# Kernel tuning notes

Hardware: AMD Instinct MI355X
Metric: run time of the kernel (lower is better)

The kernel has to match this reference:

```python
import jax, jax.numpy as jnp
import numpy as np

T, D, N, K, V = 4, 1024, 256, 64, 32000
SGLD_A, SGLD_B, SGLD_C = 0.01, 1.0, 0.55
PHI_VAR, ETA_VAR = 1.0, 1.0
ZERO = 1e-6

def jax_exp(x):
    return jnp.clip(jnp.exp(jnp.clip(x, -700.0, 700.0)), ZERO)

def setup_inputs() -> dict:
    key = jax.random.key(0)
    ks = jax.random.split(key, 13)
    W = jax.random.randint(ks[0], (T, D, N), 0, V, dtype=jnp.int32)
    Z = jax.random.randint(ks[1], (T, D, N), 0, K - 1, dtype=jnp.int32)
    prop_word_idx = jax.random.randint(ks[2], (T, D, N), 0, N, dtype=jnp.int32)
    prop_topic = jax.random.randint(ks[3], (T, D, N), 0, K - 1, dtype=jnp.int32)
    u_mh = jax.random.uniform(ks[4], (T, D, N, 2), dtype=jnp.float32)
    noise_eta = jax.random.normal(ks[5], (T, D), dtype=jnp.float32)
    noise_phi = jax.random.normal(ks[6], (T,), dtype=jnp.float32)
    alpha = jax.random.normal(ks[7], (T, K), dtype=jnp.float32)
    phi = jax.random.normal(ks[8], (T, V, K), dtype=jnp.float32) * 0.1
    eta = jax.random.normal(ks[9], (T, D, K), dtype=jnp.float32) * 0.1
    CDK = jax.random.uniform(ks[10], (T, D, K), dtype=jnp.float32) * (N / K)
    CWK = jax.random.uniform(ks[11], (T, V, K), dtype=jnp.float32)
    CK = jax.random.uniform(ks[12], (T, K), dtype=jnp.float32) * (D * N / K)
    return dict(W=W, Z=Z, prop_word_idx=prop_word_idx, prop_topic=prop_topic,
                u_mh=u_mh, noise_eta=noise_eta, noise_phi=noise_phi,
                alpha=alpha, phi=phi, eta=eta, CDK=CDK, CWK=CWK, CK=CK)

def reference(W, Z, prop_word_idx, prop_topic, u_mh, noise_eta, noise_phi,
              alpha, phi, eta, CDK, CWK, CK):
    eps = SGLD_A * (SGLD_B + 0.0) ** (-SGLD_C)  # SGLD step at iteration 0

    # --- SGLD update of eta (per doc), vmapped over (T, D) via broadcasting ---
    prior_eta = (alpha[:, None, :] - eta) / ETA_VAR                 # [T,D,K]
    grad_eta = CDK - N * jax.nn.softmax(eta, axis=-1)               # [T,D,K]
    eta_new = eta + eps / 2 * (grad_eta + prior_eta) + noise_eta[..., None] * eps

    tt = jnp.arange(T)[:, None, None]   # [T,1,1]
    dd = jnp.arange(D)[None, :, None]   # [1,D,1]

    # --- MH step 1: word-proposal (acceptance via phi ratio) ---
    pre = Z                                                           # [T,D,N]
    prop1 = jnp.take_along_axis(Z, prop_word_idx, axis=2)             # [T,D,N]
    a1 = jax_exp(phi[tt, W, prop1]) / jax_exp(phi[tt, W, pre])
    k1 = jnp.where(u_mh[..., 0] < a1, prop1, pre)

    # --- MH step 2: topic-proposal (acceptance via eta ratio) ---
    a2 = jax_exp(eta_new[tt, dd, prop_topic]) / jax_exp(eta_new[tt, dd, k1])
    z_new = jnp.where(u_mh[..., 1] < a2, prop_topic, k1)              # [T,D,N]

    # --- scatter counter updates (add new assignment, remove old) ---
    CDK_new = CDK.at[tt, dd, z_new].add(1.0).at[tt, dd, Z].add(-1.0)
    CWK_new = CWK.at[tt, W, z_new].add(1.0).at[tt, W, Z].add(-1.0)
    CK_new = CK.at[tt, z_new].add(1.0).at[tt, Z].add(-1.0)

    # --- SGLD update of phi: sequential over T (reads updated phi[t-1]) ---
    rows = [phi[t] for t in range(T)]   # each [V,K]
    phi_sigma = 1.0 / (1.0 / 100.0 + 1.0 / PHI_VAR)
    for t in range(T):
        if t == 0:
            prior = (2.0 * phi[1] * (phi_sigma / PHI_VAR) - 2.0 * rows[0]) / PHI_VAR
        elif t == T - 1:
            prior = (rows[t - 1] - rows[t]) / PHI_VAR
        else:
            prior = (phi[t + 1] + rows[t - 1] - 2.0 * rows[t]) / PHI_VAR
        grad = CWK_new[t] - CK_new[t][None, :] * jax.nn.softmax(rows[t], axis=0)
        rows[t] = rows[t] + eps / 2 * (grad + prior) + noise_phi[t] * eps
    phi_new = jnp.stack(rows)

    return (eta_new, phi_new, CDK_new, CWK_new, CK_new, z_new)
```

## Files before the change

### kernel.cpp

```cpp
#include <hip/hip_runtime.h>

#define T 4
#define D 1024
#define NN 256
#define K 64
#define V 32000
#define VK (V*K)
#define TD (T*D)

__device__ __forceinline__ float jexp(float x) {
    x = fminf(fmaxf(x, -700.0f), 700.0f);
    return fmaxf(expf(x), 1e-6f);
}


__global__ void fused_kernel(const int* __restrict__ W, const int* __restrict__ Z,
                             const int* __restrict__ pwi, const int* __restrict__ ptop,
                             const float* __restrict__ u, const float* __restrict__ phi,
                             const float* __restrict__ eta,
                             const float* __restrict__ alpha,
                             const float* __restrict__ noise_eta,
                             const float* __restrict__ CDK,
                             const float* __restrict__ CK,
                             float* __restrict__ S_part,
                             float* __restrict__ CK_new,
                             float* __restrict__ eta_new,
                             float* __restrict__ CDK_new,
                             unsigned int* __restrict__ plus,
                             unsigned int* __restrict__ minus,
                             float* __restrict__ z_out)
{
    int blk = blockIdx.x;
    int n = threadIdx.x;

    __shared__ float sm[256];
    __shared__ float esh[K];
    __shared__ int   hist[K];

    if (blk < 500) {
        if (blk == 0) CK_new[n] = CK[n];
        int t = blk / 125;
        int vbase = (blk % 125) * 256;
        int k = n & 63;
        int rr = n >> 6;
        const float* base = phi + (size_t)t * VK;
        float s = 0.0f;
        #pragma unroll 4
        for (int it = 0; it < 64; ++it) {
            int v = vbase + it * 4 + rr;
            s += expf(base[v * K + k]);
        }
        sm[n] = s;
        __syncthreads();
        if (n < 64) {
            S_part[blk * 64 + n] = sm[n] + sm[n + 64] +
                                   sm[n + 128] + sm[n + 192];
        }
        return;
    }

    int b = blk - 500;
    int r = ((b & 7) << 9) | (b >> 3);
    int t = r >> 10;
;
    int w     = W[r * NN + n];
    int pre   = Z[r * NN + n];
    int pw    = pwi[r * NN + n];
    int prop1 = Z[r * NN + pw];
    int pt    = ptop[r * NN + n];
    float2 uu = ((const float2*)u)[(size_t)r * NN + n];

    const float* prow = phi + ((size_t)t * V + w) * K;
    float f1 = prow[prop1];
    float f0 = prow[pre];

    float cdk = 0.0f;
    if (n < 64) {
        float x = eta[r * K + n];
        float m = x;
        #pragma unroll
        for (int off = 32; off >= 1; off >>= 1)
            m = fmaxf(m, __shfl_xor(m, off, 64));
        float e = expf(x - m);
        float s = e;
        #pragma unroll
        for (int off = 32; off >= 1; off >>= 1)
            s += __shfl_xor(s, off, 64);
        float smx = e / s;
        cdk = CDK[r * K + n];
        float grad  = cdk - (float)NN * smx;
        float prior = alpha[t * K + n] - x;
        float en = x + 0.005f * (grad + prior) + noise_eta[r] * 0.01f;
        esh[n] = en;
        eta_new[r * K + n] = en;
    } else if (n < 128) {
        hist[n - 64] = 0;
    }
    __syncthreads();

    float a1 = jexp(f1) / jexp(f0);
    int k1 = (uu.x < a1) ? prop1 : pre;

    float a2 = jexp(esh[pt]) / jexp(esh[k1]);
    int z = (uu.y < a2) ? pt : k1;

    atomicAdd(&hist[z], 1);
    atomicAdd(&hist[pre], -1);
    __syncthreads();

    z_out[r * NN + n] = (float)z;
    if (z != pre) {
        size_t rowbase = ((size_t)t * V + w) * 16;
        atomicAdd(&plus [rowbase + (z   >> 2)], 1u << ((z   & 3) * 8));
        atomicAdd(&minus[rowbase + (pre >> 2)], 1u << ((pre & 3) * 8));
    }
    if (n < K) {
        CDK_new[r * K + n] = cdk + (float)hist[n];
    }
}

__global__ void reduce_kernel(const float* __restrict__ S_part,
                              const float* __restrict__ CDKn,
                              const float* __restrict__ CDK,
                              float* __restrict__ S,
                              float* __restrict__ CK_new)
{
    int b = blockIdx.x;
    int tid = threadIdx.x;

    if (b < 4 && tid < 64) {
        float s = 0.0f;
        #pragma unroll 5
        for (int i = 0; i < 125; ++i)
            s += S_part[(b * 125 + i) * 64 + tid];
        S[b * 64 + tid] = s;
    }

    int t  = b >> 4;
    int k  = tid & 63;
    int dl = tid >> 6;
    int dbase = (b & 15) << 6;
    float s = 0.0f;
    #pragma unroll
    for (int i = 0; i < 16; ++i) {
        int d = dbase + dl + (i << 2);
        size_t idx = ((size_t)(t << 10) + d) * 64 + k;
        s += CDKn[idx] - CDK[idx];
    }
    __shared__ float sm[256];
    sm[tid] = s;
    __syncthreads();
    if (tid < 64) {
        float tot = sm[k] + sm[k + 64] + sm[k + 128] + sm[k + 192];
        if (tot != 0.0f) atomicAdd(&CK_new[(t << 6) + k], tot);
    }
}

__global__ void phi_update_kernel(const float* __restrict__ phi,
                                  const float* __restrict__ CWK,
                                  const unsigned int* __restrict__ plus,
                                  const unsigned int* __restrict__ minus,
                                  const float* __restrict__ CKn,
                                  const float* __restrict__ S,
                                  const float* __restrict__ noise_phi,
                                  float* __restrict__ phi_new,
                                  float* __restrict__ CWK_new)
{
    int i4 = blockIdx.x * 256 + threadIdx.x;
    int kg = i4 & 15;
    const float eps = 0.01f;
    const float half_eps = 0.005f;
    const float sig = 1.0f / 1.01f;

    const float4* phi4  = (const float4*)phi;
    const float4* cwk4  = (const float4*)CWK;
    const float4* ck4   = (const float4*)CKn;
    const float4* s4    = (const float4*)S;
    float4*       out4  = (float4*)phi_new;
    float4*       cwkn4 = (float4*)CWK_new;

    float4 p0 = phi4[i4];
    float4 p1 = phi4[i4 +     512000];
    float4 p2 = phi4[i4 + 2 * 512000];
    float4 p3 = phi4[i4 + 3 * 512000];

    float4 c0 = cwk4[i4];
    float4 c1 = cwk4[i4 +     512000];
    float4 c2 = cwk4[i4 + 2 * 512000];
    float4 c3 = cwk4[i4 + 3 * 512000];

    unsigned int pl0 = plus [i4],               mi0 = minus[i4];
    unsigned int pl1 = plus [i4 +     512000],  mi1 = minus[i4 +     512000];
    unsigned int pl2 = plus [i4 + 2 * 512000],  mi2 = minus[i4 + 2 * 512000];
    unsigned int pl3 = plus [i4 + 3 * 512000],  mi3 = minus[i4 + 3 * 512000];

    float4 ckn0 = ck4[kg],      ckn1 = ck4[16 + kg];
    float4 ckn2 = ck4[32 + kg], ckn3 = ck4[48 + kg];
    float4 ss0 = s4[kg],        ss1 = s4[16 + kg];
    float4 ss2 = s4[32 + kg],   ss3 = s4[48 + kg];

    float np0 = noise_phi[0] * eps, np1 = noise_phi[1] * eps;
    float np2 = noise_phi[2] * eps, np3 = noise_phi[3] * eps;

    float4 o0, o1, o2, o3, w0, w1, w2, w3;
    #pragma unroll
    for (int j = 0; j < 4; ++j) {
        int sh = j * 8;
        float q0 = (&p0.x)[j], q1 = (&p1.x)[j], q2 = (&p2.x)[j], q3 = (&p3.x)[j];
        float d0 = (float)((pl0 >> sh) & 255u) - (float)((mi0 >> sh) & 255u);
        float d1 = (float)((pl1 >> sh) & 255u) - (float)((mi1 >> sh) & 255u);
        float d2 = (float)((pl2 >> sh) & 255u) - (float)((mi2 >> sh) & 255u);
        float d3 = (float)((pl3 >> sh) & 255u) - (float)((mi3 >> sh) & 255u);
        float cw0 = (&c0.x)[j] + d0;
        float cw1 = (&c1.x)[j] + d1;
        float cw2 = (&c2.x)[j] + d2;
        float cw3 = (&c3.x)[j] + d3;
        (&w0.x)[j] = cw0; (&w1.x)[j] = cw1; (&w2.x)[j] = cw2; (&w3.x)[j] = cw3;

        float g0 = cw0 - (&ckn0.x)[j] * (expf(q0) / (&ss0.x)[j]);
        float g1 = cw1 - (&ckn1.x)[j] * (expf(q1) / (&ss1.x)[j]);
        float g2 = cw2 - (&ckn2.x)[j] * (expf(q2) / (&ss2.x)[j]);
        float g3 = cw3 - (&ckn3.x)[j] * (expf(q3) / (&ss3.x)[j]);

        float r0 = q0 + half_eps * (g0 + 2.0f * q1 * sig - 2.0f * q0) + np0;
        float r1 = q1 + half_eps * (g1 + q2 + r0 - 2.0f * q1)         + np1;
        float r2 = q2 + half_eps * (g2 + q3 + r1 - 2.0f * q2)         + np2;
        float r3 = q3 + half_eps * (g3 + r2 - q3)                      + np3;

        (&o0.x)[j] = r0; (&o1.x)[j] = r1; (&o2.x)[j] = r2; (&o3.x)[j] = r3;
    }

    out4[i4]              = o0;
    out4[i4 +     512000] = o1;
    out4[i4 + 2 * 512000] = o2;
    out4[i4 + 3 * 512000] = o3;

    cwkn4[i4]              = w0;
    cwkn4[i4 +     512000] = w1;
    cwkn4[i4 + 2 * 512000] = w2;
    cwkn4[i4 + 3 * 512000] = w3;
}

extern "C" void kernel_launch(void* const* d_in, const int* in_sizes, int n_in,
                              void* d_out, int out_size, void* d_ws, size_t ws_size,
                              hipStream_t stream)
{
    const int*   W         = (const int*)  d_in[0];
    const int*   Z         = (const int*)  d_in[1];
    const int*   pwi       = (const int*)  d_in[2];
    const int*   ptop      = (const int*)  d_in[3];
    const float* u_mh      = (const float*)d_in[4];
    const float* noise_eta = (const float*)d_in[5];
    const float* noise_phi = (const float*)d_in[6];
    const float* alpha     = (const float*)d_in[7];
    const float* phi       = (const float*)d_in[8];
    const float* eta       = (const float*)d_in[9];
    const float* CDK       = (const float*)d_in[10];
    const float* CWK       = (const float*)d_in[11];
    const float* CK        = (const float*)d_in[12];

    float* out     = (float*)d_out;
    float* eta_new = out;
    float* phi_new = out + 262144;
    float* CDK_new = out + 8454144;
    float* CWK_new = out + 8716288;
    float* CK_new  = out + 16908288;
    float* z_out   = out + 16908544;

    float* ws      = (float*)d_ws;
    float* S       = ws;
    float* S_part  = ws + 256;
    unsigned int* plus  = (unsigned int*)(ws + 256 + 32000);
    unsigned int* minus = plus + 2048000;

    hipMemsetAsync(plus, 0, 2 * (size_t)VK * sizeof(unsigned int) / 1, stream) ;

    fused_kernel<<<500 + TD, 256, 0, stream>>>(W, Z, pwi, ptop, u_mh, phi,
                                               eta, alpha, noise_eta, CDK, CK,
                                               S_part, CK_new,
                                               eta_new, CDK_new, plus, minus, z_out);
    reduce_kernel<<<64, 256, 0, stream>>>(S_part, CDK_new, CDK, S, CK_new);
    phi_update_kernel<<<VK / 1024, 256, 0, stream>>>(phi, CWK, plus, minus,
                                                     CK_new, S, noise_phi,
                                                     phi_new, CWK_new);
}
```

Measured before the change: 265.1 us.

## Replace dense global scatter histograms with bucketed lists and LDS histogram kernel

```diff
diff --git a/kernel.cpp b/kernel.cpp
--- a/kernel.cpp
+++ b/kernel.cpp
@@ -7,6 +7,7 @@
 #define V 32000
 #define VK (V*K)
 #define TD (T*D)
+#define CAP 4096
 
 __device__ __forceinline__ float jexp(float x) {
     x = fminf(fmaxf(x, -700.0f), 700.0f);
@@ -26,8 +27,8 @@
                              float* __restrict__ CK_new,
                              float* __restrict__ eta_new,
                              float* __restrict__ CDK_new,
-                             unsigned int* __restrict__ plus,
-                             unsigned int* __restrict__ minus,
+                             unsigned int* __restrict__ resv,
+                             unsigned int* __restrict__ list,
                              float* __restrict__ z_out)
 {
     int blk = blockIdx.x;
@@ -36,6 +37,8 @@
     __shared__ float sm[256];
     __shared__ float esh[K];
     __shared__ int   hist[K];
+    __shared__ int   bcnt[8];
+    __shared__ int   bbase[8];
 
     if (blk < 500) {
         if (blk == 0) CK_new[n] = CK[n];
@@ -62,7 +65,8 @@
     int b = blk - 500;
     int r = ((b & 7) << 9) | (b >> 3);
     int t = r >> 10;
-;
+    int slice = (b >> 3) & 15;
+
     int w     = W[r * NN + n];
     int pre   = Z[r * NN + n];
     int pw    = pwi[r * NN + n];
@@ -95,6 +99,8 @@
         eta_new[r * K + n] = en;
     } else if (n < 128) {
         hist[n - 64] = 0;
+    } else if (n < 136) {
+        bcnt[n - 128] = 0;
     }
     __syncthreads();
 
@@ -106,16 +112,74 @@
 
     atomicAdd(&hist[z], 1);
     atomicAdd(&hist[pre], -1);
+
+    int keep = (z != pre);
+    int bucket = w / 4000;
+    int myidx = 0;
+    if (keep) myidx = atomicAdd(&bcnt[bucket], 1);
+    __syncthreads();
+
+    if (n < 8) {
+        bbase[n] = (int)atomicAdd(&resv[(t * 8 + n) * 16 + slice],
+                                  (unsigned int)bcnt[n]);
+    }
     __syncthreads();
 
     z_out[r * NN + n] = (float)z;
-    if (z != pre) {
-        size_t rowbase = ((size_t)t * V + w) * 16;
-        atomicAdd(&plus [rowbase + (z   >> 2)], 1u << ((z   & 3) * 8));
-        atomicAdd(&minus[rowbase + (pre >> 2)], 1u << ((pre & 3) * 8));
+    if (keep) {
+        int slot = bbase[bucket] + myidx;
+        if (slot < CAP) {
+            unsigned int pk = (unsigned int)w | ((unsigned int)z << 15) |
+                              ((unsigned int)pre << 21);
+            list[(size_t)((t * 8 + bucket) * 16 + slice) * CAP + slot] = pk;
+        }
     }
     if (n < K) {
         CDK_new[r * K + n] = cdk + (float)hist[n];
+    }
+}
+
+__global__ void cwk_kernel(const unsigned int* __restrict__ list,
+                           const unsigned int* __restrict__ resv,
+                           const float* __restrict__ CWK,
+                           float* __restrict__ CWK_new)
+{
+    int blk = blockIdx.x;
+    int t      = blk >> 6;
+    int bucket = (blk >> 3) & 7;
+    int eighth = blk & 7;
+    int vbase  = bucket * 4000 + eighth * 500;
+
+    __shared__ unsigned int plusH[8000];
+    __shared__ unsigned int minusH[8000];
+    for (int i = threadIdx.x; i < 8000; i += 256) { plusH[i] = 0u; minusH[i] = 0u; }
+    __syncthreads();
+
+    int segbase = (t * 8 + bucket) * 16;
+    for (int s = 0; s < 16; ++s) {
+        int len = (int)resv[segbase + s]; if (len > CAP) len = CAP;
+        const unsigned int* lp = list + (size_t)(segbase + s) * CAP;
+        for (int i = threadIdx.x; i < len; i += 256) {
+            unsigned int pk = lp[i];
+            int wv = (int)(pk & 32767u);
+            unsigned int vl = (unsigned int)(wv - vbase);
+            if (vl < 500u) {
+                int z  = (int)((pk >> 15) & 63u);
+                int pr = (int)((pk >> 21) & 63u);
+                atomicAdd(&plusH [vl * 16 + (z  >> 2)], 1u << ((z  & 3) * 8));
+                atomicAdd(&minusH[vl * 16 + (pr >> 2)], 1u << ((pr & 3) * 8));
+            }
+        }
+    }
+    __syncthreads();
+
+    const float* src = CWK     + ((size_t)t * V + vbase) * 64;
+    float*       dst = CWK_new + ((size_t)t * V + vbase) * 64;
+    for (int idx = threadIdx.x; idx < 500 * 64; idx += 256) {
+        int v = idx >> 6, k = idx & 63, sh = (k & 3) * 8;
+        float d = (float)((plusH [v * 16 + (k >> 2)] >> sh) & 255u)
+                - (float)((minusH[v * 16 + (k >> 2)] >> sh) & 255u);
+        dst[idx] = src[idx] + d;
     }
 }
 
@@ -157,14 +221,11 @@
 }
 
 __global__ void phi_update_kernel(const float* __restrict__ phi,
-                                  const float* __restrict__ CWK,
-                                  const unsigned int* __restrict__ plus,
-                                  const unsigned int* __restrict__ minus,
+                                  const float* __restrict__ CWKn,
                                   const float* __restrict__ CKn,
                                   const float* __restrict__ S,
                                   const float* __restrict__ noise_phi,
-                                  float* __restrict__ phi_new,
-                                  float* __restrict__ CWK_new)
+                                  float* __restrict__ phi_new)
 {
     int i4 = blockIdx.x * 256 + threadIdx.x;
     int kg = i4 & 15;
@@ -173,11 +234,10 @@
     const float sig = 1.0f / 1.01f;
 
     const float4* phi4  = (const float4*)phi;
-    const float4* cwk4  = (const float4*)CWK;
+    const float4* cwk4  = (const float4*)CWKn;
     const float4* ck4   = (const float4*)CKn;
     const float4* s4    = (const float4*)S;
     float4*       out4  = (float4*)phi_new;
-    float4*       cwkn4 = (float4*)CWK_new;
 
     float4 p0 = phi4[i4];
     float4 p1 = phi4[i4 +     512000];
@@ -189,11 +249,6 @@
     float4 c2 = cwk4[i4 + 2 * 512000];
     float4 c3 = cwk4[i4 + 3 * 512000];
 
-    unsigned int pl0 = plus [i4],               mi0 = minus[i4];
-    unsigned int pl1 = plus [i4 +     512000],  mi1 = minus[i4 +     512000];
-    unsigned int pl2 = plus [i4 + 2 * 512000],  mi2 = minus[i4 + 2 * 512000];
-    unsigned int pl3 = plus [i4 + 3 * 512000],  mi3 = minus[i4 + 3 * 512000];
-
     float4 ckn0 = ck4[kg],      ckn1 = ck4[16 + kg];
     float4 ckn2 = ck4[32 + kg], ckn3 = ck4[48 + kg];
     float4 ss0 = s4[kg],        ss1 = s4[16 + kg];
@@ -202,25 +257,14 @@
     float np0 = noise_phi[0] * eps, np1 = noise_phi[1] * eps;
     float np2 = noise_phi[2] * eps, np3 = noise_phi[3] * eps;
 
-    float4 o0, o1, o2, o3, w0, w1, w2, w3;
+    float4 o0, o1, o2, o3;
     #pragma unroll
     for (int j = 0; j < 4; ++j) {
-        int sh = j * 8;
         float q0 = (&p0.x)[j], q1 = (&p1.x)[j], q2 = (&p2.x)[j], q3 = (&p3.x)[j];
-        float d0 = (float)((pl0 >> sh) & 255u) - (float)((mi0 >> sh) & 255u);
-        float d1 = (float)((pl1 >> sh) & 255u) - (float)((mi1 >> sh) & 255u);
-        float d2 = (float)((pl2 >> sh) & 255u) - (float)((mi2 >> sh) & 255u);
-        float d3 = (float)((pl3 >> sh) & 255u) - (float)((mi3 >> sh) & 255u);
-        float cw0 = (&c0.x)[j] + d0;
-        float cw1 = (&c1.x)[j] + d1;
-        float cw2 = (&c2.x)[j] + d2;
-        float cw3 = (&c3.x)[j] + d3;
-        (&w0.x)[j] = cw0; (&w1.x)[j] = cw1; (&w2.x)[j] = cw2; (&w3.x)[j] = cw3;
-
-        float g0 = cw0 - (&ckn0.x)[j] * (expf(q0) / (&ss0.x)[j]);
-        float g1 = cw1 - (&ckn1.x)[j] * (expf(q1) / (&ss1.x)[j]);
-        float g2 = cw2 - (&ckn2.x)[j] * (expf(q2) / (&ss2.x)[j]);
-        float g3 = cw3 - (&ckn3.x)[j] * (expf(q3) / (&ss3.x)[j]);
+        float g0 = (&c0.x)[j] - (&ckn0.x)[j] * (expf(q0) / (&ss0.x)[j]);
+        float g1 = (&c1.x)[j] - (&ckn1.x)[j] * (expf(q1) / (&ss1.x)[j]);
+        float g2 = (&c2.x)[j] - (&ckn2.x)[j] * (expf(q2) / (&ss2.x)[j]);
+        float g3 = (&c3.x)[j] - (&ckn3.x)[j] * (expf(q3) / (&ss3.x)[j]);
 
         float r0 = q0 + half_eps * (g0 + 2.0f * q1 * sig - 2.0f * q0) + np0;
         float r1 = q1 + half_eps * (g1 + q2 + r0 - 2.0f * q1)         + np1;
@@ -234,11 +278,6 @@
     out4[i4 +     512000] = o1;
     out4[i4 + 2 * 512000] = o2;
     out4[i4 + 3 * 512000] = o3;
-
-    cwkn4[i4]              = w0;
-    cwkn4[i4 +     512000] = w1;
-    cwkn4[i4 + 2 * 512000] = w2;
-    cwkn4[i4 + 3 * 512000] = w3;
 }
 
 extern "C" void kernel_launch(void* const* d_in, const int* in_sizes, int n_in,
@@ -270,17 +309,17 @@
     float* ws      = (float*)d_ws;
     float* S       = ws;
     float* S_part  = ws + 256;
-    unsigned int* plus  = (unsigned int*)(ws + 256 + 32000);
-    unsigned int* minus = plus + 2048000;
-
-    hipMemsetAsync(plus, 0, 2 * (size_t)VK * sizeof(unsigned int) / 1, stream) ;
+    unsigned int* resv = (unsigned int*)(ws + 256 + 32000);
+    unsigned int* list = resv + 512;
+
+    hipMemsetAsync(resv, 0, 512 * sizeof(unsigned int), stream);
 
     fused_kernel<<<500 + TD, 256, 0, stream>>>(W, Z, pwi, ptop, u_mh, phi,
                                                eta, alpha, noise_eta, CDK, CK,
                                                S_part, CK_new,
-                                               eta_new, CDK_new, plus, minus, z_out);
+                                               eta_new, CDK_new, resv, list, z_out);
+    cwk_kernel<<<256, 256, 0, stream>>>(list, resv, CWK, CWK_new);
     reduce_kernel<<<64, 256, 0, stream>>>(S_part, CDK_new, CDK, S, CK_new);
-    phi_update_kernel<<<VK / 1024, 256, 0, stream>>>(phi, CWK, plus, minus,
-                                                     CK_new, S, noise_phi,
-                                                     phi_new, CWK_new);
-}
+    phi_update_kernel<<<VK / 1024, 256, 0, stream>>>(phi, CWK_new, CK_new, S,
+                                                     noise_phi, phi_new);
+}
```

Result: slower. 275.0 us (+3.7%).
